# Performance work log

Measured on AMD Instinct MI355X. Metric: run time of the kernel, lower is better.

## Reference

```python
import jax, jax.numpy as jnp
import numpy as np

IN_F, OUT_F = 4096, 11008
TOKENS = 8

def setup_inputs() -> dict:
    key = jax.random.key(0)
    k1, k2, k3, k4, k5, k6 = jax.random.split(key, 6)
    x = jax.random.normal(k1, (TOKENS, IN_F), dtype=jnp.float32)
    base_weight = jax.random.normal(k2, (OUT_F, IN_F), dtype=jnp.float32) * 0.02
    q_delta = jax.random.randint(k3, (OUT_F, IN_F), 0, 16, dtype=jnp.int32)
    scales = jax.random.uniform(k4, (OUT_F,), dtype=jnp.float32) * 1e-3 + 1e-8
    zero_points = jax.random.normal(k5, (OUT_F,), dtype=jnp.float32)
    bias = jax.random.normal(k6, (OUT_F,), dtype=jnp.float32) * 0.01
    return {"x": x, "base_weight": base_weight, "q_delta": q_delta,
            "scales": scales, "zero_points": zero_points, "bias": bias}

def reference(x, base_weight, q_delta, scales, zero_points, bias):
    # per-channel dequantize: delta[o,i] = (q[o,i] - zp[o]) * scale[o]
    delta = (q_delta.astype(jnp.float32) - zero_points[:, None]) * scales[:, None]
    w = base_weight + delta  # [out, in]
    return jnp.dot(x, w.T) + bias  # [tokens, out]
```

## Files before the change

### kernel.cpp

```cpp
#include <hip/hip_runtime.h>


#define IN_F    4096
#define OUT_F   11008
#define TOKENS  8
#define RPB     8
#define THREADS 256
#define NBLOCKS (OUT_F / RPB)

typedef float vf4 __attribute__((ext_vector_type(4)));
typedef int   vi4 __attribute__((ext_vector_type(4)));

__global__ __launch_bounds__(THREADS, 2)
void DeltaQuantLinear_87540023427416_kernel(
    const float* __restrict__ x,
    const float* __restrict__ w,
    const int*   __restrict__ q,
    const float* __restrict__ scales,
    const float* __restrict__ zps,
    const float* __restrict__ bias,
    float*       __restrict__ out)
{
    __shared__ float lds[32 * 257];
    __shared__ float lds2[32 * 8];

    const int tid = threadIdx.x;
    const int o0  = blockIdx.x * RPB;

    float s[RPB], c0[RPB];
#pragma unroll
    for (int r = 0; r < RPB; ++r) {
        const float sc = scales[o0 + r];
        s[r]  = sc;
        c0[r] = -zps[o0 + r] * sc;
    }

    float acc[RPB][TOKENS];
#pragma unroll
    for (int r = 0; r < RPB; ++r)
#pragma unroll
        for (int t = 0; t < TOKENS; ++t) acc[r][t] = 0.0f;

#pragma unroll
    for (int c = 0; c < 4; ++c) {
        const int kbase = c * 1024 + tid * 4;

        vf4 xr[TOKENS];
#pragma unroll
        for (int t = 0; t < TOKENS; ++t)
            xr[t] = *(const vf4*)(x + t * IN_F + kbase);

#pragma unroll
        for (int g = 0; g < 2; ++g) {
            vf4 wv[4];
            vi4 qv[4];
#pragma unroll
            for (int rr = 0; rr < 4; ++rr) {
                const int r = g * 4 + rr;
                const float* wp = w + (size_t)(o0 + r) * IN_F + kbase;
                const int*   qp = q + (size_t)(o0 + r) * IN_F + kbase;
                wv[rr] = __builtin_nontemporal_load((const vf4*)wp);
                qv[rr] = __builtin_nontemporal_load((const vi4*)qp);
            }
#pragma unroll
            for (int rr = 0; rr < 4; ++rr) {
                const int r = g * 4 + rr;
#pragma unroll
                for (int j = 0; j < 4; ++j) {
                    const float wfull = fmaf((float)qv[rr][j], s[r], wv[rr][j] + c0[r]);
#pragma unroll
                    for (int t = 0; t < TOKENS; ++t) {
                        acc[r][t] = fmaf(xr[t][j], wfull, acc[r][t]);
                    }
                }
            }
        }
    }

#pragma unroll
    for (int h = 0; h < 2; ++h) {
#pragma unroll
        for (int rl = 0; rl < 4; ++rl)
#pragma unroll
            for (int t = 0; t < TOKENS; ++t)
                lds[(rl * 8 + t) * 257 + tid] = acc[h * 4 + rl][t];
        __syncthreads();

        {
            const int l = tid & 31;
            const int p = tid >> 5;
            float sum = 0.0f;
            const float* row = &lds[l * 257 + p * 32];
#pragma unroll
            for (int j = 0; j < 32; ++j) sum += row[j];
            lds2[l * 8 + p] = sum;
        }
        __syncthreads();

        if (tid < 32) {
            float tot = 0.0f;
#pragma unroll
            for (int j = 0; j < 8; ++j) tot += lds2[tid * 8 + j];
            const int rl = tid >> 3;
            const int t  = tid & 7;
            const int o  = o0 + h * 4 + rl;
            out[t * OUT_F + o] = tot + bias[o];
        }
        __syncthreads();
    }
}

extern "C" void kernel_launch(void* const* d_in, const int* in_sizes, int n_in,
                              void* d_out, int out_size, void* d_ws, size_t ws_size,
                              hipStream_t stream) {
    const float* x      = (const float*)d_in[0];
    const float* w      = (const float*)d_in[1];
    const int*   q      = (const int*)d_in[2];
    const float* scales = (const float*)d_in[3];
    const float* zps    = (const float*)d_in[4];
    const float* bias   = (const float*)d_in[5];
    float* out = (float*)d_out;

    DeltaQuantLinear_87540023427416_kernel<<<NBLOCKS, THREADS, 0, stream>>>(
        x, w, q, scales, zps, bias, out);
}
```

Measured before the change: 337.7 us.

## Use single-wave blocks over four rows with a shuffle-based reduction

Each block is now a single 64-lane wave that owns four output rows and walks the full K dimension in 16 slices. Before, 256-thread blocks owned eight rows and split K across threads, then reduced through LDS with three barriers. The cross-lane reduction is now an xor-shuffle butterfly, which removes shared memory and __syncthreads entirely. The block count doubles, and the launch bound asks for higher occupancy so more loads stay in flight. The trade-off is a longer serial K loop per wave and a redundant full butterfly in which every lane computes every sum. The final store also indexes the accumulator array dynamically, which may turn into select chains or spill to scratch.

```diff
diff --git a/kernel.cpp b/kernel.cpp
--- a/kernel.cpp
+++ b/kernel.cpp
@@ -4,14 +4,15 @@
 #define IN_F    4096
 #define OUT_F   11008
 #define TOKENS  8
-#define RPB     8
-#define THREADS 256
-#define NBLOCKS (OUT_F / RPB)
+#define RPW     4
+#define THREADS 64
+#define NBLOCKS (OUT_F / RPW)
+#define KSLICE  (IN_F / (64 * 4))
 
 typedef float vf4 __attribute__((ext_vector_type(4)));
 typedef int   vi4 __attribute__((ext_vector_type(4)));
 
-__global__ __launch_bounds__(THREADS, 2)
+__global__ __launch_bounds__(THREADS, 3)
 void DeltaQuantLinear_87540023427416_kernel(
     const float* __restrict__ x,
     const float* __restrict__ w,
@@ -21,92 +22,69 @@
     const float* __restrict__ bias,
     float*       __restrict__ out)
 {
-    __shared__ float lds[32 * 257];
-    __shared__ float lds2[32 * 8];
+    const int lane = threadIdx.x;
+    const int r0   = blockIdx.x * RPW;
 
-    const int tid = threadIdx.x;
-    const int o0  = blockIdx.x * RPB;
-
-    float s[RPB], c0[RPB];
+    float s[RPW], c0[RPW];
 #pragma unroll
-    for (int r = 0; r < RPB; ++r) {
-        const float sc = scales[o0 + r];
+    for (int r = 0; r < RPW; ++r) {
+        const float sc = scales[r0 + r];
         s[r]  = sc;
-        c0[r] = -zps[o0 + r] * sc;
+        c0[r] = -zps[r0 + r] * sc;
     }
 
-    float acc[RPB][TOKENS];
+    float acc[RPW][TOKENS];
 #pragma unroll
-    for (int r = 0; r < RPB; ++r)
+    for (int r = 0; r < RPW; ++r)
 #pragma unroll
         for (int t = 0; t < TOKENS; ++t) acc[r][t] = 0.0f;
 
+#pragma unroll 2
+    for (int sl = 0; sl < KSLICE; ++sl) {
+        const int k = sl * 256 + lane * 4;
+
+        vf4 wv[RPW];
+        vi4 qv[RPW];
 #pragma unroll
-    for (int c = 0; c < 4; ++c) {
-        const int kbase = c * 1024 + tid * 4;
+        for (int r = 0; r < RPW; ++r) {
+            const float* wp = w + (size_t)(r0 + r) * IN_F + k;
+            const int*   qp = q + (size_t)(r0 + r) * IN_F + k;
+            wv[r] = __builtin_nontemporal_load((const vf4*)wp);
+            qv[r] = __builtin_nontemporal_load((const vi4*)qp);
+        }
 
         vf4 xr[TOKENS];
 #pragma unroll
         for (int t = 0; t < TOKENS; ++t)
-            xr[t] = *(const vf4*)(x + t * IN_F + kbase);
+            xr[t] = *(const vf4*)(x + t * IN_F + k);
 
 #pragma unroll
-        for (int g = 0; g < 2; ++g) {
-            vf4 wv[4];
-            vi4 qv[4];
+        for (int r = 0; r < RPW; ++r) {
 #pragma unroll
-            for (int rr = 0; rr < 4; ++rr) {
-                const int r = g * 4 + rr;
-                const float* wp = w + (size_t)(o0 + r) * IN_F + kbase;
-                const int*   qp = q + (size_t)(o0 + r) * IN_F + kbase;
-                wv[rr] = __builtin_nontemporal_load((const vf4*)wp);
-                qv[rr] = __builtin_nontemporal_load((const vi4*)qp);
-            }
+            for (int j = 0; j < 4; ++j) {
+                const float wfull = fmaf((float)qv[r][j], s[r], wv[r][j] + c0[r]);
 #pragma unroll
-            for (int rr = 0; rr < 4; ++rr) {
-                const int r = g * 4 + rr;
-#pragma unroll
-                for (int j = 0; j < 4; ++j) {
-                    const float wfull = fmaf((float)qv[rr][j], s[r], wv[rr][j] + c0[r]);
-#pragma unroll
-                    for (int t = 0; t < TOKENS; ++t) {
-                        acc[r][t] = fmaf(xr[t][j], wfull, acc[r][t]);
-                    }
-                }
+                for (int t = 0; t < TOKENS; ++t)
+                    acc[r][t] = fmaf(xr[t][j], wfull, acc[r][t]);
             }
         }
     }
 
 #pragma unroll
-    for (int h = 0; h < 2; ++h) {
+    for (int i = 0; i < 6; ++i) {
+        const int mask = 1 << i;
 #pragma unroll
-        for (int rl = 0; rl < 4; ++rl)
+        for (int r = 0; r < RPW; ++r)
 #pragma unroll
             for (int t = 0; t < TOKENS; ++t)
-                lds[(rl * 8 + t) * 257 + tid] = acc[h * 4 + rl][t];
-        __syncthreads();
+                acc[r][t] += __shfl_xor(acc[r][t], mask, 64);
+    }
 
-        {
-            const int l = tid & 31;
-            const int p = tid >> 5;
-            float sum = 0.0f;
-            const float* row = &lds[l * 257 + p * 32];
-#pragma unroll
-            for (int j = 0; j < 32; ++j) sum += row[j];
-            lds2[l * 8 + p] = sum;
-        }
-        __syncthreads();
-
-        if (tid < 32) {
-            float tot = 0.0f;
-#pragma unroll
-            for (int j = 0; j < 8; ++j) tot += lds2[tid * 8 + j];
-            const int rl = tid >> 3;
-            const int t  = tid & 7;
-            const int o  = o0 + h * 4 + rl;
-            out[t * OUT_F + o] = tot + bias[o];
-        }
-        __syncthreads();
+    if (lane < RPW * TOKENS) {
+        const int r = lane & (RPW - 1);
+        const int t = lane >> 2;
+        const int o = r0 + r;
+        out[t * OUT_F + o] = acc[r][t] + bias[o];
     }
 }
 
```

New measurement: 369.4 us. 9.4% more time.
